# Kernel tuning notes

Measured on AMD Instinct MI355X. Metric: run time of the kernel, lower is better.

## Reference

```python
import jax, jax.numpy as jnp
import numpy as np

B, NQ, NK = 8, 1024, 1024
DQ = DK = DV = 512
H = 8
DH = DV // H
EPS = 1e-5
NEG = -1e9


def _layer_norm(x, g, b):
    mu = jnp.mean(x, axis=-1, keepdims=True)
    var = jnp.mean(jnp.square(x - mu), axis=-1, keepdims=True)
    return (x - mu) * jax.lax.rsqrt(var + EPS) * g + b


def setup_inputs() -> dict:
    key = jax.random.key(0)
    ks = jax.random.split(key, 16)
    s_q = 1.0 / np.sqrt(DQ)
    s_k = 1.0 / np.sqrt(DK)
    s_v = 1.0 / np.sqrt(DV)
    return {
        "Q": jax.random.normal(ks[0], (B, NQ, DQ), jnp.float32),
        "K": jax.random.normal(ks[1], (B, NK, DK), jnp.float32),
        "mask": jax.random.randint(ks[2], (B, NK), 0, 2, jnp.int32),
        "Wq": jax.random.uniform(ks[3], (DQ, DV), jnp.float32, -s_q, s_q),
        "bq": jax.random.uniform(ks[4], (DV,), jnp.float32, -s_q, s_q),
        "Wk": jax.random.uniform(ks[5], (DK, DV), jnp.float32, -s_k, s_k),
        "bk": jax.random.uniform(ks[6], (DV,), jnp.float32, -s_k, s_k),
        "Wv": jax.random.uniform(ks[7], (DK, DV), jnp.float32, -s_k, s_k),
        "bv": jax.random.uniform(ks[8], (DV,), jnp.float32, -s_k, s_k),
        "Wo": jax.random.uniform(ks[9], (DV, DV), jnp.float32, -s_v, s_v),
        "bo": jax.random.uniform(ks[10], (DV,), jnp.float32, -s_v, s_v),
        "g0": jnp.ones((DV,), jnp.float32),
        "b0": jnp.zeros((DV,), jnp.float32),
        "g1": jnp.ones((DV,), jnp.float32),
        "b1": jnp.zeros((DV,), jnp.float32),
    }


def reference(Q, K, mask, Wq, bq, Wk, bk, Wv, bv, Wo, bo, g0, b0, g1, b1):
    b = Q.shape[0]
    # projections: [B, N, DV] -> [B, N, H, DH]
    q = (Q @ Wq + bq).reshape(b, -1, H, DH)
    k = (K @ Wk + bk).reshape(b, -1, H, DH)
    v = (K @ Wv + bv).reshape(b, -1, H, DH)
    scores = jnp.einsum("bqhd,bkhd->bhqk", q, k) / np.sqrt(DH)  # [B,H,Nq,Nk]
    scores = jnp.where((mask == 0)[:, None, None, :], NEG, scores)
    A = jax.nn.softmax(scores, axis=-1)
    o = q + jnp.einsum("bhqk,bkhd->bqhd", A, v)  # residual on projected Q (per head)
    O = o.reshape(b, -1, DV)
    O = _layer_norm(O, g0, b0)
    O = O + jax.nn.relu(O @ Wo + bo)
    O = _layer_norm(O, g1, b1)
    return O
```

## Files before the change

kernel.cpp:

```cpp
#include <hip/hip_runtime.h>


typedef float f32x4 __attribute__((ext_vector_type(4)));
typedef short bf16x8 __attribute__((ext_vector_type(8)));
typedef unsigned short u16;

#define MFMA16 __builtin_amdgcn_mfma_f32_16x16x32_bf16

__device__ __forceinline__ float bf2f(u16 u){
    unsigned x = ((unsigned)u) << 16;
    return __builtin_bit_cast(float, x);
}
__device__ __forceinline__ u16 f2bf(float f){
    unsigned u = __builtin_bit_cast(unsigned, f);
    u = u + 0x7fffu + ((u >> 16) & 1u);
    return (u16)(u >> 16);
}

__device__ __forceinline__ void gload_lds16(const u16* g, u16* l){
    __builtin_amdgcn_global_load_lds(
        (const __attribute__((address_space(1))) void*)g,
        (__attribute__((address_space(3))) void*)l, 16, 0, 0);
}

__global__ __launch_bounds__(256) void transpose_w(
    const float* __restrict__ Wq, const float* __restrict__ Wk,
    const float* __restrict__ Wv, const float* __restrict__ Wo,
    u16* __restrict__ wt)
{
    const int z = blockIdx.z;
    const float* W = (z == 0) ? Wq : (z == 1) ? Wk : (z == 2) ? Wv : Wo;
    u16* out = wt + (size_t)z * 512 * 512;

    __shared__ u16 tile[32][33];
    const int k0 = blockIdx.y * 32, n0 = blockIdx.x * 32;
    const int c = threadIdx.x & 31, r = threadIdx.x >> 5;
#pragma unroll
    for (int i = 0; i < 4; i++) {
        int rr = r + i * 8;
        tile[rr][c] = f2bf(W[(size_t)(k0 + rr) * 512 + n0 + c]);
    }
    __syncthreads();
#pragma unroll
    for (int i = 0; i < 4; i++) {
        int rr = r + i * 8;
        out[(size_t)(n0 + rr) * 512 + k0 + c] = tile[c][rr];
    }
}

__global__ __launch_bounds__(256) void transpose_v(
    const u16* __restrict__ vb, u16* __restrict__ vtg)
{
    __shared__ u16 tile[32][33];
    const int bh = blockIdx.z;
    const int b = bh >> 3, h = bh & 7;
    const int k0 = blockIdx.x * 32, d0 = blockIdx.y * 32;
    const int c = threadIdx.x & 31, r = threadIdx.x >> 5;
#pragma unroll
    for (int i = 0; i < 4; i++) {
        int rr = r + i * 8;
        tile[rr][c] = vb[(size_t)(b * 1024 + k0 + rr) * 512 + h * 64 + d0 + c];
    }
    __syncthreads();
#pragma unroll
    for (int i = 0; i < 4; i++) {
        int rr = r + i * 8;
        vtg[(size_t)(bh * 64 + d0 + rr) * 1024 + k0 + c] = tile[c][rr];
    }
}

__global__ __launch_bounds__(256) void gemm_proj(
    const float* __restrict__ Q, const float* __restrict__ K,
    const u16* __restrict__ wt,
    const float* __restrict__ bq, const float* __restrict__ bk, const float* __restrict__ bv,
    u16* __restrict__ qb, u16* __restrict__ kb, u16* __restrict__ vb)
{
    __shared__ __align__(16) u16 lds_a[128 * 40];
    __shared__ __align__(16) u16 lds_b[128 * 32];

    const int f = blockIdx.x + (blockIdx.y << 2) + (blockIdx.z << 8);
    const int xcd = f & 7, s = f >> 3;
    const int z = s >> 5;
    const int r_ = s & 31;
    const int bm = xcd * 8 + (r_ >> 2);
    const int bn = r_ & 3;

    const float* X = (z == 0) ? Q : K;
    const u16* Wt = wt + (size_t)z * 512 * 512;
    const float* bias = (z == 0) ? bq : (z == 1) ? bk : bv;
    u16* outb = (z == 0) ? qb : (z == 1) ? kb : vb;

    const int t = threadIdx.x;
    const int wave = t >> 6, lane = t & 63, quad = lane >> 4, lm = lane & 15;
    const int wm = wave >> 1, wn = wave & 1;

    const u16* bsrc[2];
    u16* bdst[2];
#pragma unroll
    for (int j = 0; j < 2; j++) {
        const int r = j * 64 + wave * 16 + (lane >> 2);
        const int cg = ((lane & 3) ^ (r & 3)) * 8;
        bsrc[j] = &Wt[(size_t)(bn * 128 + r) * 512 + cg];
        bdst[j] = &lds_b[(j * 2048) + wave * 512];
    }

    f32x4 acc[4][4];
    const f32x4 zz = {0.f, 0.f, 0.f, 0.f};
#pragma unroll
    for (int i = 0; i < 4; i++)
#pragma unroll
        for (int j = 0; j < 4; j++) acc[i][j] = zz;

    for (int k0 = 0; k0 < 512; k0 += 32) {
        gload_lds16(bsrc[0] + k0, bdst[0]);
        gload_lds16(bsrc[1] + k0, bdst[1]);
#pragma unroll
        for (int i = 0; i < 2; i++) {
            int idx = t + i * 256;
            int r = idx >> 2, c = (idx & 3) * 8;
            const float* xp = &X[(size_t)(bm * 128 + r) * 512 + k0 + c];
            f32x4 a0 = *(const f32x4*)xp;
            f32x4 a1 = *(const f32x4*)(xp + 4);
            bf16x8 xv;
#pragma unroll
            for (int j = 0; j < 4; j++) { xv[j] = (short)f2bf(a0[j]); xv[4 + j] = (short)f2bf(a1[j]); }
            *(bf16x8*)&lds_a[r * 40 + c] = xv;
        }
        __syncthreads();
        bf16x8 af[4], bfr[4];
#pragma unroll
        for (int mi = 0; mi < 4; mi++)
            af[mi] = *(const bf16x8*)&lds_a[(wm * 64 + mi * 16 + lm) * 40 + quad * 8];
#pragma unroll
        for (int ni = 0; ni < 4; ni++)
            bfr[ni] = *(const bf16x8*)&lds_b[(wn * 64 + ni * 16 + lm) * 32
                                            + ((quad ^ (lm & 3)) * 8)];
#pragma unroll
        for (int mi = 0; mi < 4; mi++)
#pragma unroll
            for (int ni = 0; ni < 4; ni++)
                acc[mi][ni] = MFMA16(af[mi], bfr[ni], acc[mi][ni], 0, 0, 0);
        __syncthreads();
    }

#pragma unroll
    for (int mi = 0; mi < 4; mi++) {
#pragma unroll
        for (int ni = 0; ni < 4; ni++) {
            const int col = bn * 128 + wn * 64 + ni * 16 + lm;
            const float bv_ = bias[col];
#pragma unroll
            for (int r = 0; r < 4; r++) {
                const int row = bm * 128 + wm * 64 + mi * 16 + quad * 4 + r;
                outb[(size_t)row * 512 + col] = f2bf(acc[mi][ni][r] + bv_);
            }
        }
    }
}

__global__ __launch_bounds__(256) void gemm_mlp(
    const u16* __restrict__ X, const u16* __restrict__ wt,
    const float* __restrict__ bo, const float* __restrict__ resid,
    float* __restrict__ outf)
{
    __shared__ __align__(16) u16 lds_a[128 * 32];
    __shared__ __align__(16) u16 lds_b[128 * 32];

    const u16* Wt = wt + (size_t)3 * 512 * 512;

    const int f = blockIdx.x + (blockIdx.y << 2);
    const int xcd = f & 7, s = f >> 3;
    const int bm = xcd * 8 + (s >> 2);
    const int bn = s & 3;

    const int t = threadIdx.x;
    const int wave = t >> 6, lane = t & 63, quad = lane >> 4, lm = lane & 15;
    const int wm = wave >> 1, wn = wave & 1;

    const u16* asrc[2];
    const u16* bsrc[2];
    u16* adst[2];
    u16* bdst[2];
#pragma unroll
    for (int j = 0; j < 2; j++) {
        const int r = j * 64 + wave * 16 + (lane >> 2);
        const int cg = ((lane & 3) ^ (r & 3)) * 8;
        asrc[j] = &X [(size_t)(bm * 128 + r) * 512 + cg];
        bsrc[j] = &Wt[(size_t)(bn * 128 + r) * 512 + cg];
        adst[j] = &lds_a[(j * 2048) + wave * 512];
        bdst[j] = &lds_b[(j * 2048) + wave * 512];
    }

    f32x4 acc[4][4];
    const f32x4 zz = {0.f, 0.f, 0.f, 0.f};
#pragma unroll
    for (int i = 0; i < 4; i++)
#pragma unroll
        for (int j = 0; j < 4; j++) acc[i][j] = zz;

    for (int k0 = 0; k0 < 512; k0 += 32) {
        gload_lds16(asrc[0] + k0, adst[0]);
        gload_lds16(asrc[1] + k0, adst[1]);
        gload_lds16(bsrc[0] + k0, bdst[0]);
        gload_lds16(bsrc[1] + k0, bdst[1]);
        __syncthreads();
        bf16x8 af[4], bfr[4];
        const int cxor = (quad ^ (lm & 3)) * 8;
#pragma unroll
        for (int mi = 0; mi < 4; mi++)
            af[mi] = *(const bf16x8*)&lds_a[(wm * 64 + mi * 16 + lm) * 32 + cxor];
#pragma unroll
        for (int ni = 0; ni < 4; ni++)
            bfr[ni] = *(const bf16x8*)&lds_b[(wn * 64 + ni * 16 + lm) * 32 + cxor];
#pragma unroll
        for (int mi = 0; mi < 4; mi++)
#pragma unroll
            for (int ni = 0; ni < 4; ni++)
                acc[mi][ni] = MFMA16(af[mi], bfr[ni], acc[mi][ni], 0, 0, 0);
        __syncthreads();
    }

#pragma unroll
    for (int mi = 0; mi < 4; mi++) {
#pragma unroll
        for (int ni = 0; ni < 4; ni++) {
            const int col = bn * 128 + wn * 64 + ni * 16 + lm;
            const float bv_ = bo[col];
#pragma unroll
            for (int r = 0; r < 4; r++) {
                const int row = bm * 128 + wm * 64 + mi * 16 + quad * 4 + r;
                const size_t off = (size_t)row * 512 + col;
                outf[off] = resid[off] + fmaxf(acc[mi][ni][r] + bv_, 0.f);
            }
        }
    }
}

__global__ __launch_bounds__(256, 4) void attn_kernel(
    const u16* __restrict__ qb, const u16* __restrict__ kb, const u16* __restrict__ vtg,
    const int* __restrict__ mask, float* __restrict__ O)
{
    __shared__ __align__(16) u16 k_tile[64 * 88];
    __shared__ __align__(16) u16 vt[64 * 88];
    __shared__ __align__(16) u16 p_st[4 * 16 * 88];

    const int i = blockIdx.x;
    const int s_ = i >> 3;
    const int bh = (i & 7) + 8 * (s_ >> 4);
    const int qt = s_ & 15;
    const int b = bh >> 3, h = bh & 7;

    const int t = threadIdx.x, wave = t >> 6, lane = t & 63;
    const int quad = lane >> 4, lm = lane & 15;
    const int qbase = qt * 64 + wave * 16;
    const size_t baseb = (size_t)b * 1024 * 512;
    const size_t vbase = (size_t)((b * 8 + h) * 64) * 1024;
    const int* mrow = &mask[b * 1024];

    bf16x8 aq[2];
#pragma unroll
    for (int ks = 0; ks < 2; ks++)
        aq[ks] = *(const bf16x8*)&qb[baseb +
            (size_t)(qbase + lm) * 512 + h * 64 + ks * 32 + quad * 8];

    float lsum[4] = {0.f, 0.f, 0.f, 0.f};
    f32x4 oacc[4];
    const f32x4 zz = {0.f, 0.f, 0.f, 0.f};
#pragma unroll
    for (int c = 0; c < 4; c++) oacc[c] = zz;

    const float SC2 = 0.125f * 1.44269504088896341f;
    const int srow = t >> 2, scol = (t & 3) * 16;
    u16* pw = &p_st[wave * 16 * 88];

    const u16* kgp = &kb[baseb + (size_t)srow * 512 + h * 64 + scol];
    const u16* vgp = &vtg[vbase + (size_t)srow * 1024 + scol];

    bf16x8 kA0, kA1, vA0, vA1, kB0, kB1, vB0, vB1;

    auto load_t = [&](int kt, bf16x8& k0, bf16x8& k1, bf16x8& v0, bf16x8& v1) {
        const u16* kp = kgp + (size_t)kt * 64 * 512;
        k0 = *(const bf16x8*)kp;
        k1 = *(const bf16x8*)(kp + 8);
        const u16* vp = vgp + kt * 64;
        v0 = *(const bf16x8*)vp;
        v1 = *(const bf16x8*)(vp + 8);
    };
    auto store_t = [&](bf16x8 k0, bf16x8 k1, bf16x8 v0, bf16x8 v1) {
        *(bf16x8*)&k_tile[srow * 88 + scol]     = k0;
        *(bf16x8*)&k_tile[srow * 88 + scol + 8] = k1;
        *(bf16x8*)&vt[srow * 88 + scol]     = v0;
        *(bf16x8*)&vt[srow * 88 + scol + 8] = v1;
    };

    auto compute_t = [&](int kt) {
        const int keyg = kt * 64;
        float bias_n[4];
#pragma unroll
        for (int n = 0; n < 4; n++)
            bias_n[n] = mrow[keyg + n * 16 + lm] ? 0.0f : -30000.0f;

        bf16x8 bk[4][2];
#pragma unroll
        for (int n = 0; n < 4; n++)
#pragma unroll
            for (int ks = 0; ks < 2; ks++)
                bk[n][ks] = *(const bf16x8*)&k_tile[(n * 16 + lm) * 88 + ks * 32 + quad * 8];

#pragma unroll
        for (int n = 0; n < 4; n++) {
            f32x4 S = zz;
            __builtin_amdgcn_s_setprio(1);
            S = MFMA16(aq[0], bk[n][0], S, 0, 0, 0);
            S = MFMA16(aq[1], bk[n][1], S, 0, 0, 0);
            __builtin_amdgcn_s_setprio(0);
#pragma unroll
            for (int r = 0; r < 4; r++) {
                float p = __builtin_amdgcn_exp2f(__builtin_fmaf(S[r], SC2, bias_n[n]));
                lsum[r] += p;
                pw[(quad * 4 + r) * 88 + n * 16 + lm] = f2bf(p);
            }
        }

#pragma unroll
        for (int ks = 0; ks < 2; ks++) {
            bf16x8 ap = *(const bf16x8*)&pw[lm * 88 + ks * 32 + quad * 8];
            __builtin_amdgcn_s_setprio(1);
#pragma unroll
            for (int c = 0; c < 4; c++) {
                bf16x8 bv_ = *(const bf16x8*)&vt[(c * 16 + lm) * 88 + ks * 32 + quad * 8];
                oacc[c] = MFMA16(ap, bv_, oacc[c], 0, 0, 0);
            }
            __builtin_amdgcn_s_setprio(0);
        }
    };

    load_t(0, kA0, kA1, vA0, vA1);

    for (int kt = 0; kt < 16; kt += 2) {
        store_t(kA0, kA1, vA0, vA1);
        load_t(kt + 1, kB0, kB1, vB0, vB1);
        __syncthreads();
        compute_t(kt);
        __syncthreads();
        store_t(kB0, kB1, vB0, vB1);
        load_t((kt + 2) & 15, kA0, kA1, vA0, vA1);
        __syncthreads();
        compute_t(kt + 1);
        __syncthreads();
    }

#pragma unroll
    for (int r = 0; r < 4; r++) {
        float s = lsum[r];
        s += __shfl_xor(s, 1); s += __shfl_xor(s, 2);
        s += __shfl_xor(s, 4); s += __shfl_xor(s, 8);
        lsum[r] = s;
    }

#pragma unroll
    for (int c = 0; c < 4; c++)
#pragma unroll
        for (int r = 0; r < 4; r++) {
            const int row = qbase + quad * 4 + r;
            const int d = h * 64 + c * 16 + lm;
            const size_t off = baseb + (size_t)row * 512 + d;
            O[off] = bf2f(qb[off]) + oacc[c][r] / lsum[r];
        }
}

__global__ __launch_bounds__(256) void ln_kernel(
    const float* __restrict__ in, const float* __restrict__ g, const float* __restrict__ bsh,
    u16* __restrict__ outb, float* __restrict__ outf)
{
    const int row = blockIdx.x * 4 + (threadIdx.x >> 6);
    const int lane = threadIdx.x & 63;
    const float* x = in + (size_t)row * 512 + lane * 8;
    float v[8];
    *(f32x4*)&v[0] = *(const f32x4*)&x[0];
    *(f32x4*)&v[4] = *(const f32x4*)&x[4];
    float s = 0.f, sq = 0.f;
#pragma unroll
    for (int j = 0; j < 8; j++) { s += v[j]; sq += v[j] * v[j]; }
#pragma unroll
    for (int off = 1; off < 64; off <<= 1) {
        s += __shfl_xor(s, off);
        sq += __shfl_xor(sq, off);
    }
    const float mu = s * (1.f / 512.f);
    const float var = sq * (1.f / 512.f) - mu * mu;
    const float rs = rsqrtf(var + 1e-5f);
    float y[8];
#pragma unroll
    for (int j = 0; j < 8; j++) {
        int col = lane * 8 + j;
        y[j] = (v[j] - mu) * rs * g[col] + bsh[col];
    }
    if (outb != nullptr) {
        bf16x8 ov;
#pragma unroll
        for (int j = 0; j < 8; j++) ov[j] = (short)f2bf(y[j]);
        *(bf16x8*)&outb[(size_t)row * 512 + lane * 8] = ov;
    }
    if (outf != nullptr) {
        float* o = outf + (size_t)row * 512 + lane * 8;
        *(f32x4*)&o[0] = *(const f32x4*)&y[0];
        *(f32x4*)&o[4] = *(const f32x4*)&y[4];
    }
}

extern "C" void kernel_launch(void* const* d_in, const int* in_sizes, int n_in,
                              void* d_out, int out_size, void* d_ws, size_t ws_size,
                              hipStream_t stream) {
    const float* Q  = (const float*)d_in[0];
    const float* K  = (const float*)d_in[1];
    const int* mask = (const int*)d_in[2];
    const float* Wq = (const float*)d_in[3];
    const float* bq = (const float*)d_in[4];
    const float* Wk = (const float*)d_in[5];
    const float* bk = (const float*)d_in[6];
    const float* Wv = (const float*)d_in[7];
    const float* bv = (const float*)d_in[8];
    const float* Wo = (const float*)d_in[9];
    const float* bo = (const float*)d_in[10];
    const float* g0 = (const float*)d_in[11];
    const float* b0 = (const float*)d_in[12];
    const float* g1 = (const float*)d_in[13];
    const float* b1 = (const float*)d_in[14];
    float* out = (float*)d_out;

    char* ws = (char*)d_ws;
    const size_t MB = 1048576;
    u16*   wt  = (u16*)(ws);
    u16*   qb  = (u16*)(ws + 2 * MB);
    u16*   kb  = (u16*)(ws + 10 * MB);
    u16*   vtg = (u16*)(ws + 18 * MB);
    u16*   vb  = (u16*)(ws + 26 * MB);
    float* Of  = (float*)(ws + 26 * MB);
    u16*   O1b = (u16*)(ws + 2 * MB);
    float* O1f = (float*)(ws + 10 * MB);
    float* Uf  = (float*)(ws + 26 * MB);

    transpose_w<<<dim3(16, 16, 4), 256, 0, stream>>>(Wq, Wk, Wv, Wo, wt);
    gemm_proj<<<dim3(4, 64, 3), 256, 0, stream>>>(Q, K, wt, bq, bk, bv, qb, kb, vb);
    transpose_v<<<dim3(32, 2, 64), 256, 0, stream>>>(vb, vtg);
    attn_kernel<<<1024, 256, 0, stream>>>(qb, kb, vtg, mask, Of);
    ln_kernel<<<2048, 256, 0, stream>>>(Of, g0, b0, O1b, O1f);
    gemm_mlp<<<dim3(4, 64, 1), 256, 0, stream>>>(O1b, wt, bo, O1f, Uf);
    ln_kernel<<<2048, 256, 0, stream>>>(Uf, g1, b1, nullptr, out);
}
```

Baseline: 202.5 us.

## Fuse K and V projections sharing A tile; shrink MLP GEMM N-tile

The projection GEMM now computes the K and V projections in the same block, so the fp32 K input is loaded and converted to bf16 once and reused for both weight matrices. The grid drops from 768 to 512 blocks, with Q blocks doing one GEMM and K blocks doing two, which makes the work per block uneven and adds registers for a second accumulator set. The MLP GEMM switches from 128x128 to 128x64 tiles with 512 blocks, giving more blocks to fill the CUs at the cost of reloading the A tile more often.

Measured after the change: 224.4 us. 1.11x slower.

```diff
diff --git a/kernel.cpp b/kernel.cpp
--- a/kernel.cpp
+++ b/kernel.cpp
@@ -76,44 +76,53 @@
     u16* __restrict__ qb, u16* __restrict__ kb, u16* __restrict__ vb)
 {
     __shared__ __align__(16) u16 lds_a[128 * 40];
-    __shared__ __align__(16) u16 lds_b[128 * 32];
-
-    const int f = blockIdx.x + (blockIdx.y << 2) + (blockIdx.z << 8);
+    __shared__ __align__(16) u16 lds_b1[128 * 32];
+    __shared__ __align__(16) u16 lds_b2[128 * 32];
+
+    const int f = blockIdx.x;
     const int xcd = f & 7, s = f >> 3;
-    const int z = s >> 5;
+    const int zq = s >> 5;
     const int r_ = s & 31;
     const int bm = xcd * 8 + (r_ >> 2);
     const int bn = r_ & 3;
 
-    const float* X = (z == 0) ? Q : K;
-    const u16* Wt = wt + (size_t)z * 512 * 512;
-    const float* bias = (z == 0) ? bq : (z == 1) ? bk : bv;
-    u16* outb = (z == 0) ? qb : (z == 1) ? kb : vb;
+    const float* X = zq ? K : Q;
+    const u16* Wt1 = wt + (size_t)zq * 512 * 512;
+    const u16* Wt2 = wt + (size_t)2 * 512 * 512;
+    const float* bias1 = zq ? bk : bq;
 
     const int t = threadIdx.x;
     const int wave = t >> 6, lane = t & 63, quad = lane >> 4, lm = lane & 15;
     const int wm = wave >> 1, wn = wave & 1;
 
-    const u16* bsrc[2];
-    u16* bdst[2];
+    const u16* b1src[2];
+    const u16* b2src[2];
+    u16* b1dst[2];
+    u16* b2dst[2];
 #pragma unroll
     for (int j = 0; j < 2; j++) {
         const int r = j * 64 + wave * 16 + (lane >> 2);
         const int cg = ((lane & 3) ^ (r & 3)) * 8;
-        bsrc[j] = &Wt[(size_t)(bn * 128 + r) * 512 + cg];
-        bdst[j] = &lds_b[(j * 2048) + wave * 512];
-    }
-
-    f32x4 acc[4][4];
+        b1src[j] = &Wt1[(size_t)(bn * 128 + r) * 512 + cg];
+        b2src[j] = &Wt2[(size_t)(bn * 128 + r) * 512 + cg];
+        b1dst[j] = &lds_b1[(j * 2048) + wave * 512];
+        b2dst[j] = &lds_b2[(j * 2048) + wave * 512];
+    }
+
+    f32x4 acc1[4][4], acc2[4][4];
     const f32x4 zz = {0.f, 0.f, 0.f, 0.f};
 #pragma unroll
     for (int i = 0; i < 4; i++)
 #pragma unroll
-        for (int j = 0; j < 4; j++) acc[i][j] = zz;
+        for (int j = 0; j < 4; j++) { acc1[i][j] = zz; acc2[i][j] = zz; }
 
     for (int k0 = 0; k0 < 512; k0 += 32) {
-        gload_lds16(bsrc[0] + k0, bdst[0]);
-        gload_lds16(bsrc[1] + k0, bdst[1]);
+        gload_lds16(b1src[0] + k0, b1dst[0]);
+        gload_lds16(b1src[1] + k0, b1dst[1]);
+        if (zq) {
+            gload_lds16(b2src[0] + k0, b2dst[0]);
+            gload_lds16(b2src[1] + k0, b2dst[1]);
+        }
 #pragma unroll
         for (int i = 0; i < 2; i++) {
             int idx = t + i * 256;
@@ -131,28 +140,55 @@
 #pragma unroll
         for (int mi = 0; mi < 4; mi++)
             af[mi] = *(const bf16x8*)&lds_a[(wm * 64 + mi * 16 + lm) * 40 + quad * 8];
+        const int cxor = (quad ^ (lm & 3)) * 8;
 #pragma unroll
         for (int ni = 0; ni < 4; ni++)
-            bfr[ni] = *(const bf16x8*)&lds_b[(wn * 64 + ni * 16 + lm) * 32
-                                            + ((quad ^ (lm & 3)) * 8)];
+            bfr[ni] = *(const bf16x8*)&lds_b1[(wn * 64 + ni * 16 + lm) * 32 + cxor];
 #pragma unroll
         for (int mi = 0; mi < 4; mi++)
 #pragma unroll
             for (int ni = 0; ni < 4; ni++)
-                acc[mi][ni] = MFMA16(af[mi], bfr[ni], acc[mi][ni], 0, 0, 0);
-        __syncthreads();
-    }
-
+                acc1[mi][ni] = MFMA16(af[mi], bfr[ni], acc1[mi][ni], 0, 0, 0);
+        if (zq) {
+            bf16x8 bfv[4];
+#pragma unroll
+            for (int ni = 0; ni < 4; ni++)
+                bfv[ni] = *(const bf16x8*)&lds_b2[(wn * 64 + ni * 16 + lm) * 32 + cxor];
+#pragma unroll
+            for (int mi = 0; mi < 4; mi++)
+#pragma unroll
+                for (int ni = 0; ni < 4; ni++)
+                    acc2[mi][ni] = MFMA16(af[mi], bfv[ni], acc2[mi][ni], 0, 0, 0);
+        }
+        __syncthreads();
+    }
+
+    u16* out1 = zq ? kb : qb;
 #pragma unroll
     for (int mi = 0; mi < 4; mi++) {
 #pragma unroll
         for (int ni = 0; ni < 4; ni++) {
             const int col = bn * 128 + wn * 64 + ni * 16 + lm;
-            const float bv_ = bias[col];
+            const float b1_ = bias1[col];
 #pragma unroll
             for (int r = 0; r < 4; r++) {
                 const int row = bm * 128 + wm * 64 + mi * 16 + quad * 4 + r;
-                outb[(size_t)row * 512 + col] = f2bf(acc[mi][ni][r] + bv_);
+                out1[(size_t)row * 512 + col] = f2bf(acc1[mi][ni][r] + b1_);
+            }
+        }
+    }
+    if (zq) {
+#pragma unroll
+        for (int mi = 0; mi < 4; mi++) {
+#pragma unroll
+            for (int ni = 0; ni < 4; ni++) {
+                const int col = bn * 128 + wn * 64 + ni * 16 + lm;
+                const float b2_ = bv[col];
+#pragma unroll
+                for (int r = 0; r < 4; r++) {
+                    const int row = bm * 128 + wm * 64 + mi * 16 + quad * 4 + r;
+                    vb[(size_t)row * 512 + col] = f2bf(acc2[mi][ni][r] + b2_);
+                }
             }
         }
     }
@@ -164,58 +200,61 @@
     float* __restrict__ outf)
 {
     __shared__ __align__(16) u16 lds_a[128 * 32];
-    __shared__ __align__(16) u16 lds_b[128 * 32];
+    __shared__ __align__(16) u16 lds_b[64 * 32];
 
     const u16* Wt = wt + (size_t)3 * 512 * 512;
 
-    const int f = blockIdx.x + (blockIdx.y << 2);
+    const int f = blockIdx.x;
     const int xcd = f & 7, s = f >> 3;
-    const int bm = xcd * 8 + (s >> 2);
-    const int bn = s & 3;
+    const int bm = xcd * 8 + (s >> 3);
+    const int bn = s & 7;
 
     const int t = threadIdx.x;
     const int wave = t >> 6, lane = t & 63, quad = lane >> 4, lm = lane & 15;
     const int wm = wave >> 1, wn = wave & 1;
 
     const u16* asrc[2];
-    const u16* bsrc[2];
     u16* adst[2];
-    u16* bdst[2];
 #pragma unroll
     for (int j = 0; j < 2; j++) {
         const int r = j * 64 + wave * 16 + (lane >> 2);
         const int cg = ((lane & 3) ^ (r & 3)) * 8;
-        asrc[j] = &X [(size_t)(bm * 128 + r) * 512 + cg];
-        bsrc[j] = &Wt[(size_t)(bn * 128 + r) * 512 + cg];
+        asrc[j] = &X[(size_t)(bm * 128 + r) * 512 + cg];
         adst[j] = &lds_a[(j * 2048) + wave * 512];
-        bdst[j] = &lds_b[(j * 2048) + wave * 512];
-    }
-
-    f32x4 acc[4][4];
+    }
+    const u16* bsrc;
+    u16* bdst;
+    {
+        const int r = wave * 16 + (lane >> 2);
+        const int cg = ((lane & 3) ^ (r & 3)) * 8;
+        bsrc = &Wt[(size_t)(bn * 64 + r) * 512 + cg];
+        bdst = &lds_b[wave * 512];
+    }
+
+    f32x4 acc[4][2];
     const f32x4 zz = {0.f, 0.f, 0.f, 0.f};
 #pragma unroll
     for (int i = 0; i < 4; i++)
 #pragma unroll
-        for (int j = 0; j < 4; j++) acc[i][j] = zz;
+        for (int j = 0; j < 2; j++) acc[i][j] = zz;
 
     for (int k0 = 0; k0 < 512; k0 += 32) {
         gload_lds16(asrc[0] + k0, adst[0]);
         gload_lds16(asrc[1] + k0, adst[1]);
-        gload_lds16(bsrc[0] + k0, bdst[0]);
-        gload_lds16(bsrc[1] + k0, bdst[1]);
-        __syncthreads();
-        bf16x8 af[4], bfr[4];
+        gload_lds16(bsrc + k0, bdst);
+        __syncthreads();
+        bf16x8 af[4], bfr[2];
         const int cxor = (quad ^ (lm & 3)) * 8;
 #pragma unroll
         for (int mi = 0; mi < 4; mi++)
             af[mi] = *(const bf16x8*)&lds_a[(wm * 64 + mi * 16 + lm) * 32 + cxor];
 #pragma unroll
-        for (int ni = 0; ni < 4; ni++)
-            bfr[ni] = *(const bf16x8*)&lds_b[(wn * 64 + ni * 16 + lm) * 32 + cxor];
+        for (int ni = 0; ni < 2; ni++)
+            bfr[ni] = *(const bf16x8*)&lds_b[(wn * 32 + ni * 16 + lm) * 32 + cxor];
 #pragma unroll
         for (int mi = 0; mi < 4; mi++)
 #pragma unroll
-            for (int ni = 0; ni < 4; ni++)
+            for (int ni = 0; ni < 2; ni++)
                 acc[mi][ni] = MFMA16(af[mi], bfr[ni], acc[mi][ni], 0, 0, 0);
         __syncthreads();
     }
@@ -223,8 +262,8 @@
 #pragma unroll
     for (int mi = 0; mi < 4; mi++) {
 #pragma unroll
-        for (int ni = 0; ni < 4; ni++) {
-            const int col = bn * 128 + wn * 64 + ni * 16 + lm;
+        for (int ni = 0; ni < 2; ni++) {
+            const int col = bn * 64 + wn * 32 + ni * 16 + lm;
             const float bv_ = bo[col];
 #pragma unroll
             for (int r = 0; r < 4; r++) {
@@ -442,10 +481,10 @@
     float* Uf  = (float*)(ws + 26 * MB);
 
     transpose_w<<<dim3(16, 16, 4), 256, 0, stream>>>(Wq, Wk, Wv, Wo, wt);
-    gemm_proj<<<dim3(4, 64, 3), 256, 0, stream>>>(Q, K, wt, bq, bk, bv, qb, kb, vb);
+    gemm_proj<<<512, 256, 0, stream>>>(Q, K, wt, bq, bk, bv, qb, kb, vb);
     transpose_v<<<dim3(32, 2, 64), 256, 0, stream>>>(vb, vtg);
     attn_kernel<<<1024, 256, 0, stream>>>(qb, kb, vtg, mask, Of);
     ln_kernel<<<2048, 256, 0, stream>>>(Of, g0, b0, O1b, O1f);
-    gemm_mlp<<<dim3(4, 64, 1), 256, 0, stream>>>(O1b, wt, bo, O1f, Uf);
+    gemm_mlp<<<512, 256, 0, stream>>>(O1b, wt, bo, O1f, Uf);
     ln_kernel<<<2048, 256, 0, stream>>>(Uf, g1, b1, nullptr, out);
 }
```
